# Kernel optimization log

Measured on AMD Instinct MI355X. Metric: run time of the kernel, lower is better.

Reference implementation:

```python
import jax, jax.numpy as jnp
import numpy as np

# pseudo_image_dims = [512, 512] -> canvas_x = dims[0], canvas_y = dims[1]
CANVAS_X = 512
CANVAS_Y = 512
SHIFT_SIZE = 2          # gen_index_shift(2, ...) -> 5x5 neighborhood
VR_THRESH = 0.1
B = 2
N_LI = 1_000_000
N_RA = 500_000


def setup_inputs() -> dict:
    key = jax.random.key(0)
    k1, k2, k3, k4 = jax.random.split(key, 4)
    li_input = jax.random.normal(k1, (B, N_LI, 4), dtype=jnp.float32)
    ra_input = jax.random.normal(k2, (B, N_RA, 5), dtype=jnp.float32)
    # voxel_coords (y, x) per valid point; batch column is implicitly 0
    li_coords = jax.random.randint(k3, (B, N_LI, 2), 0, CANVAS_Y).astype(jnp.int32)
    ra_coords = jax.random.randint(k4, (B, N_RA, 2), 0, CANVAS_Y).astype(jnp.int32)
    # all points valid; identity point_idxes (deterministic scatter)
    li_point_idxes = jnp.broadcast_to(jnp.arange(N_LI, dtype=jnp.int32), (B, N_LI))
    ra_point_idxes = jnp.broadcast_to(jnp.arange(N_RA, dtype=jnp.int32), (B, N_RA))
    return {
        "li_input": li_input,
        "li_coords": li_coords,
        "li_point_idxes": li_point_idxes,
        "ra_input": ra_input,
        "ra_coords": ra_coords,
        "ra_point_idxes": ra_point_idxes,
    }


def _per_batch(li_pts, li_coor, li_valid, ra_pts, ra_coor, ra_valid):
    X, Y = CANVAS_X, CANVAS_Y
    # flat BEV index per valid point: y * canvas_x + x, scattered to full point set
    li_flat = (li_coor[:, 0] * X + li_coor[:, 1]).astype(jnp.int32)
    li_ind = jnp.zeros(li_pts.shape[0], jnp.int32).at[li_valid].set(li_flat)
    ra_flat = (ra_coor[:, 0] * X + ra_coor[:, 1]).astype(jnp.int32)
    ra_ind = jnp.zeros(ra_pts.shape[0], jnp.int32).at[ra_valid].set(ra_flat)

    vr = jnp.abs(ra_pts[:, 4])
    ra_dy = vr > VR_THRESH

    # DynamicScatter(average_points=False): per-voxel MAX of |vr|; a voxel is
    # dynamic if its max |vr| > 0.1. Empty voxels -> -inf identity -> not dynamic.
    vox_max = jax.ops.segment_max(vr[ra_valid], ra_flat, num_segments=Y * X)
    dyn = (vox_max > VR_THRESH).reshape(Y, X)

    # expand each dynamic voxel to its 5x5 neighborhood with the original's
    # wrap logic: y is modded by (dims[0]+1), x by (dims[1]+1); shifted cells
    # landing on the extra row/col (== dim) are dropped.
    ys = jnp.arange(Y, dtype=jnp.int32)[:, None]   # [Y,1]
    xs = jnp.arange(X, dtype=jnp.int32)[None, :]   # [1,X]
    neigh = jnp.zeros(Y * X, dtype=jnp.int32)
    for i in range(-SHIFT_SIZE, SHIFT_SIZE + 1):
        for j in range(-SHIFT_SIZE, SHIFT_SIZE + 1):
            sy = (ys + i) % (X + 1)   # grid_size[0] = pseudo_image_dims[0] + 1
            sx = (xs + j) % (Y + 1)   # grid_size[1] = pseudo_image_dims[1] + 1
            valid = dyn & (sy < Y) & (sx < X)      # [Y,X]
            flat = sy * X + sx                      # [Y,X]
            flat = jnp.where(valid, flat, 0)
            neigh = neigh.at[flat.reshape(-1)].max(valid.reshape(-1).astype(jnp.int32))
    neigh_mask = neigh > 0          # [Y*X] bool

    li_dy = neigh_mask[li_ind]      # points with matching flat index become dynamic
    return li_dy, li_ind, ra_dy, ra_ind


def reference(li_input, li_coords, li_point_idxes, ra_input, ra_coords, ra_point_idxes):
    return jax.vmap(_per_batch)(li_input, li_coords, li_point_idxes,
                                ra_input, ra_coords, ra_point_idxes)
```

## Files before the change

### kernel.cpp

```cpp
#include <hip/hip_runtime.h>

#define CANVAS 512
#define PLANE (CANVAS * CANVAS)
#define WORDS_PB 8192
#define GRIDW 513
#define BATCH 2
#define N_LI 1000000
#define N_RA 500000

typedef int int2v __attribute__((ext_vector_type(2)));
typedef int int4v __attribute__((ext_vector_type(4)));

__global__ __launch_bounds__(256) void ra_kernel(
        const float* __restrict__ ra_input,
        const int*   __restrict__ ra_coords,
        int* __restrict__ ra_dy_out,
        int* __restrict__ ra_ind_out,
        unsigned char* __restrict__ dyn) {
    int i = blockIdx.x * blockDim.x + threadIdx.x;
    if (i >= BATCH * N_RA / 2) return;
    int4v c = ((const int4v*)ra_coords)[i];
    float vr0 = fabsf(ra_input[(size_t)i * 10 + 4]);
    float vr1 = fabsf(ra_input[(size_t)i * 10 + 9]);
    int flat0 = c.x * CANVAS + c.y;
    int flat1 = c.z * CANVAS + c.w;
    int dy0 = vr0 > 0.1f ? 1 : 0;
    int dy1 = vr1 > 0.1f ? 1 : 0;

    int2v dyv;  dyv.x = dy0;   dyv.y = dy1;
    int2v indv; indv.x = flat0; indv.y = flat1;
    __builtin_nontemporal_store(dyv,  (int2v*)ra_dy_out + i);
    __builtin_nontemporal_store(indv, (int2v*)ra_ind_out + i);

    int b = i / (N_RA / 2);
    unsigned char* db = dyn + (size_t)b * PLANE;
    if (dy0) db[flat0] = 1;
    if (dy1) db[flat1] = 1;
}

__global__ __launch_bounds__(256) void dilate_kernel(
        const unsigned char* __restrict__ dyn,
        uint32_t* __restrict__ neighw) {
    int idx  = blockIdx.x * blockDim.x + threadIdx.x;
    int b    = idx >> 18;
    int cell = idx & (PLANE - 1);
    int ty = cell >> 9;
    int tx = cell & (CANVAS - 1);
    const unsigned char* d = dyn + (size_t)b * PLANE;

    int acc = 0;
#pragma unroll
    for (int off = -2; off <= 2; ++off) {
        int sy = ty - off;
        sy += (sy < 0)      ? GRIDW : 0;
        sy -= (sy >= GRIDW) ? GRIDW : 0;
        bool vy = (sy < CANVAS);
        int rowbase = (vy ? sy : 0) * CANVAS;
#pragma unroll
        for (int off2 = -2; off2 <= 2; ++off2) {
            int sx = tx - off2;
            sx += (sx < 0)      ? GRIDW : 0;
            sx -= (sx >= GRIDW) ? GRIDW : 0;
            bool vx = (sx < CANVAS);
            int v = d[rowbase + (vx ? sx : 0)];
            acc |= (vy && vx) ? v : 0;
        }
    }
    unsigned long long m = __ballot((acc & 1) != 0);
    int lane = threadIdx.x & 63;
    if (lane == 0)       neighw[idx >> 5] = (uint32_t)m;
    else if (lane == 32) neighw[idx >> 5] = (uint32_t)(m >> 32);
}

__global__ __launch_bounds__(256) void li_kernel(
        const int* __restrict__ li_coords,
        const uint32_t* __restrict__ neighw,
        int* __restrict__ li_dy_out,
        int* __restrict__ li_ind_out) {
    int i = blockIdx.x * blockDim.x + threadIdx.x;
    if (i >= BATCH * N_LI / 2) return;
    int4v c = ((const int4v*)li_coords)[i];
    int flat0 = c.x * CANVAS + c.y;
    int flat1 = c.z * CANVAS + c.w;
    int b = i / (N_LI / 2);
    const uint32_t* nb = neighw + (size_t)b * WORDS_PB;
    uint32_t w0 = nb[flat0 >> 5];
    uint32_t w1 = nb[flat1 >> 5];
    int2v dyv;
    dyv.x = (int)((w0 >> (flat0 & 31)) & 1u);
    dyv.y = (int)((w1 >> (flat1 & 31)) & 1u);
    int2v indv; indv.x = flat0; indv.y = flat1;
    __builtin_nontemporal_store(indv, (int2v*)li_ind_out + i);
    __builtin_nontemporal_store(dyv,  (int2v*)li_dy_out + i);
}

extern "C" void kernel_launch(void* const* d_in, const int* in_sizes, int n_in,
                              void* d_out, int out_size, void* d_ws, size_t ws_size,
                              hipStream_t stream) {
    const int*   li_coords = (const int*)d_in[1];
    const float* ra_input  = (const float*)d_in[3];
    const int*   ra_coords = (const int*)d_in[4];

    int* out        = (int*)d_out;
    int* li_dy_out  = out;
    int* li_ind_out = out + (size_t)BATCH * N_LI;
    int* ra_dy_out  = out + (size_t)2 * BATCH * N_LI;
    int* ra_ind_out = out + (size_t)2 * BATCH * N_LI + (size_t)BATCH * N_RA;

    unsigned char* dyn    = (unsigned char*)d_ws;
    uint32_t*      neighw = (uint32_t*)(dyn + (size_t)BATCH * PLANE);

    const int ra_pairs = BATCH * N_RA / 2;
    ra_kernel<<<(ra_pairs + 255) / 256, 256, 0, stream>>>(
        ra_input, ra_coords, ra_dy_out, ra_ind_out, dyn);

    dilate_kernel<<<BATCH * PLANE / 256, 256, 0, stream>>>(dyn, neighw);

    const int li_pairs = BATCH * N_LI / 2;
    li_kernel<<<(li_pairs + 255) / 256, 256, 0, stream>>>(
        li_coords, neighw, li_dy_out, li_ind_out);
}
```

Baseline: 123.8 us.

## Dilate eight cells per thread with packed byte loads and bitwise ops

The dilation kernel now computes eight output cells per thread. It loads 4-byte words from the five source rows and combines them with nibble extraction and shifts, writing one byte of the bitmask. This cuts the thread count and the number of byte-granular loads by roughly eightfold. The mask format changes from 32-bit words to bytes, and li_kernel is adjusted to match. Separately, the nontemporal stores for the outputs are replaced with normal stores, which changes cache behaviour on the large output writes. The wrap-around edge handling for columns 0 and 63 is more complex and could hide correctness mistakes.

Result: slower. 126.6 us (+2.3%).

```diff
diff --git a/kernel.cpp b/kernel.cpp
--- a/kernel.cpp
+++ b/kernel.cpp
@@ -2,7 +2,7 @@
 
 #define CANVAS 512
 #define PLANE (CANVAS * CANVAS)
-#define WORDS_PB 8192
+#define NBYTES_PB 32768
 #define GRIDW 513
 #define BATCH 2
 #define N_LI 1000000
@@ -29,8 +29,8 @@
 
     int2v dyv;  dyv.x = dy0;   dyv.y = dy1;
     int2v indv; indv.x = flat0; indv.y = flat1;
-    __builtin_nontemporal_store(dyv,  (int2v*)ra_dy_out + i);
-    __builtin_nontemporal_store(indv, (int2v*)ra_ind_out + i);
+    ((int2v*)ra_dy_out)[i]  = dyv;
+    ((int2v*)ra_ind_out)[i] = indv;
 
     int b = i / (N_RA / 2);
     unsigned char* db = dyn + (size_t)b * PLANE;
@@ -38,43 +38,47 @@
     if (dy1) db[flat1] = 1;
 }
 
+__device__ __forceinline__ uint32_t nib0(uint32_t v) {
+    uint32_t t = v & 0x01010101u;
+    return (t | (t >> 7) | (t >> 14) | (t >> 21)) & 0xFu;
+}
+
 __global__ __launch_bounds__(256) void dilate_kernel(
         const unsigned char* __restrict__ dyn,
-        uint32_t* __restrict__ neighw) {
-    int idx  = blockIdx.x * blockDim.x + threadIdx.x;
-    int b    = idx >> 18;
-    int cell = idx & (PLANE - 1);
-    int ty = cell >> 9;
-    int tx = cell & (CANVAS - 1);
-    const unsigned char* d = dyn + (size_t)b * PLANE;
+        unsigned char* __restrict__ neighb) {
+    int tid = blockIdx.x * blockDim.x + threadIdx.x;
+    int b = tid >> 15;
+    int B = tid & (NBYTES_PB - 1);
+    int r = B >> 6;
+    int c = B & 63;
+    const unsigned char* base = dyn + ((size_t)b << 18);
 
-    int acc = 0;
+    uint32_t va = 0, vb = 0, vc = 0, vd = 0, vl = 0, vf = 0;
 #pragma unroll
     for (int off = -2; off <= 2; ++off) {
-        int sy = ty - off;
-        sy += (sy < 0)      ? GRIDW : 0;
-        sy -= (sy >= GRIDW) ? GRIDW : 0;
-        bool vy = (sy < CANVAS);
-        int rowbase = (vy ? sy : 0) * CANVAS;
-#pragma unroll
-        for (int off2 = -2; off2 <= 2; ++off2) {
-            int sx = tx - off2;
-            sx += (sx < 0)      ? GRIDW : 0;
-            sx -= (sx >= GRIDW) ? GRIDW : 0;
-            bool vx = (sx < CANVAS);
-            int v = d[rowbase + (vx ? sx : 0)];
-            acc |= (vy && vx) ? v : 0;
+        int rr = r - off;
+        rr += (rr < 0)      ? GRIDW : 0;
+        rr -= (rr >= GRIDW) ? GRIDW : 0;
+        if (rr < CANVAS) {
+            const uint32_t* R = (const uint32_t*)(base + rr * CANVAS);
+            if (c > 0)  va |= R[2 * c - 1];
+            vb |= R[2 * c];
+            vc |= R[2 * c + 1];
+            if (c < 63) vd |= R[2 * c + 2];
+            if (c == 0)  vl |= R[127];
+            if (c == 63) vf |= R[0];
         }
     }
-    unsigned long long m = __ballot((acc & 1) != 0);
-    int lane = threadIdx.x & 63;
-    if (lane == 0)       neighw[idx >> 5] = (uint32_t)m;
-    else if (lane == 32) neighw[idx >> 5] = (uint32_t)(m >> 32);
+    uint32_t m = nib0(va) | (nib0(vb) << 4) | (nib0(vc) << 8) | (nib0(vd) << 12);
+    if (c == 0)  m |= ((vl >> 24) & 1u) << 2;
+    if (c == 63) m |= (vf & 1u) << 13;
+    uint32_t out = ((m >> 2) | (m >> 3) | (m >> 4) | (m >> 5) | (m >> 6)) & 0xFFu;
+    neighb[tid] = (unsigned char)out;
 }
 
 __global__ __launch_bounds__(256) void li_kernel(
         const int* __restrict__ li_coords,
-        const uint32_t* __restrict__ neighw,
+        const unsigned char* __restrict__ neighb,
         int* __restrict__ li_dy_out,
         int* __restrict__ li_ind_out) {
     int i = blockIdx.x * blockDim.x + threadIdx.x;
@@ -83,15 +87,15 @@
     int flat0 = c.x * CANVAS + c.y;
     int flat1 = c.z * CANVAS + c.w;
     int b = i / (N_LI / 2);
-    const uint32_t* nb = neighw + (size_t)b * WORDS_PB;
-    uint32_t w0 = nb[flat0 >> 5];
-    uint32_t w1 = nb[flat1 >> 5];
+    const unsigned char* nb = neighb + ((size_t)b << 15);
+    unsigned v0 = nb[flat0 >> 3];
+    unsigned v1 = nb[flat1 >> 3];
     int2v dyv;
-    dyv.x = (int)((w0 >> (flat0 & 31)) & 1u);
-    dyv.y = (int)((w1 >> (flat1 & 31)) & 1u);
+    dyv.x = (int)((v0 >> (flat0 & 7)) & 1u);
+    dyv.y = (int)((v1 >> (flat1 & 7)) & 1u);
     int2v indv; indv.x = flat0; indv.y = flat1;
-    __builtin_nontemporal_store(indv, (int2v*)li_ind_out + i);
-    __builtin_nontemporal_store(dyv,  (int2v*)li_dy_out + i);
+    ((int2v*)li_ind_out)[i] = indv;
+    ((int2v*)li_dy_out)[i]  = dyv;
 }
 
 extern "C" void kernel_launch(void* const* d_in, const int* in_sizes, int n_in,
@@ -108,15 +112,15 @@
     int* ra_ind_out = out + (size_t)2 * BATCH * N_LI + (size_t)BATCH * N_RA;
 
     unsigned char* dyn    = (unsigned char*)d_ws;
-    uint32_t*      neighw = (uint32_t*)(dyn + (size_t)BATCH * PLANE);
+    unsigned char* neighb = dyn + (size_t)BATCH * PLANE;
 
     const int ra_pairs = BATCH * N_RA / 2;
     ra_kernel<<<(ra_pairs + 255) / 256, 256, 0, stream>>>(
         ra_input, ra_coords, ra_dy_out, ra_ind_out, dyn);
 
-    dilate_kernel<<<BATCH * PLANE / 256, 256, 0, stream>>>(dyn, neighw);
+    dilate_kernel<<<BATCH * NBYTES_PB / 256, 256, 0, stream>>>(dyn, neighb);
 
     const int li_pairs = BATCH * N_LI / 2;
     li_kernel<<<(li_pairs + 255) / 256, 256, 0, stream>>>(
-        li_coords, neighw, li_dy_out, li_ind_out);
+        li_coords, neighb, li_dy_out, li_ind_out);
 }
```
